# Kernel tuning notes

Measured on AMD Instinct MI355X. Metric: run time of the kernel, lower is better.

Reference implementation:

```python
import jax, jax.numpy as jnp
import numpy as np

B, L, D_MODEL = 4, 2048, 1024
D_INNER = 2 * D_MODEL
D_STATE, DT_RANK = 16, 64
Q = 32768.0  # 2^15 dyadic denominator used by the block


def _find_power_of_2_scale(var, eps=1e-9):
    v = var + eps
    scale = jnp.ones_like(v)
    for t, s in [(4.0, 0.5), (16.0, 0.25), (64.0, 0.125), (256.0, 0.0625),
                 (1024.0, 0.03125), (4096.0, 0.015625), (16384.0, 0.0078125),
                 (65536.0, 0.00390625)]:
        scale = jnp.where(v >= t, s, scale)
    scale = jnp.where(v < 1.0, 1.0, scale)
    scale = jnp.where(v < 0.25, 2.0, scale)
    scale = jnp.where(v < 0.0625, 4.0, scale)
    return scale


def _sigmoid_algebraic(z):
    return 0.5 + 0.5 * z / (1.0 + jnp.abs(z))


def _rsqrt_newton(y, num_iters=3):
    y = jnp.clip(y, 1e-6, 1e6)
    r = jnp.where(y > 16.0, 0.125, 0.5)
    r = jnp.where(y > 64.0, 0.0625, r)
    r = jnp.where(y > 256.0, 0.03125, r)
    r = jnp.where(y < 4.0, 1.0, r)
    r = jnp.where(y < 1.0, 2.0, r)
    r = jnp.where(y < 0.25, 4.0, r)
    for _ in range(num_iters):
        r = jnp.clip(r * (1.5 - 0.5 * y * r * r), 1e-6, 1e3)
    return r


def _squareplus(x):
    y = jnp.clip(x * x + 4.0, 1e-6, 1e6)
    s = jnp.clip(y * _rsqrt_newton(y), 0.0, 1e3)
    return 0.5 * (x + s)


def bitshift_norm(x, gamma, step_size):
    xc = x - x.mean(axis=-1, keepdims=True)
    var = (xc * xc).mean(axis=-1, keepdims=True)
    inv_disc = _find_power_of_2_scale(var)
    inv_diff = jax.lax.rsqrt(var + 1e-6)
    inv = inv_diff + jax.lax.stop_gradient(inv_disc - inv_diff)  # LSQ-style STE
    return xc * inv * gamma * step_size


def bitlinear(x, W):
    # 1.58-bit BitLinear: ternary weight quantization with STE
    s = jnp.mean(jnp.abs(W)) + 1e-8
    Wq = jnp.clip(jnp.round(W / s), -1.0, 1.0) * s
    Wq = W + jax.lax.stop_gradient(Wq - W)
    return x @ Wq.T


def dyadic_scan(u, decay):
    # h[t] = decay[t] * h[t-1] + (1 - decay[t]) * u[t]  (convex combination)
    a = decay
    b = (1.0 - decay) * u
    def comb(c1, c2):
        a1, b1 = c1
        a2, b2 = c2
        return a1 * a2, a2 * b1 + b2
    _, h = jax.lax.associative_scan(comb, (a, b), axis=1)
    return h


def setup_inputs() -> dict:
    key = jax.random.key(0)
    ks = jax.random.split(key, 9)
    d = {}
    d["x"] = jax.random.normal(ks[0], (B, L, D_MODEL), dtype=jnp.float32)
    d["gamma"] = jnp.ones((D_MODEL,), jnp.float32)
    d["step_size"] = jnp.ones((1,), jnp.float32)
    d["W_in"] = jax.random.normal(ks[1], (2 * D_INNER, D_MODEL), jnp.float32) * (D_MODEL ** -0.5)
    d["conv_w"] = jax.random.normal(ks[2], (D_INNER, 1, 4), jnp.float32) * 0.5
    d["conv_b"] = jnp.zeros((D_INNER,), jnp.float32)
    d["W_x"] = jax.random.normal(ks[3], (DT_RANK + 2 * D_STATE, D_INNER), jnp.float32) * (D_INNER ** -0.5)
    d["W_dt"] = jax.random.normal(ks[4], (D_INNER, DT_RANK), jnp.float32) * (DT_RANK ** -0.5)
    d["b_dt"] = jax.random.normal(ks[5], (D_INNER,), jnp.float32) * 0.1
    d["W_out"] = jax.random.normal(ks[6], (D_MODEL, D_INNER), jnp.float32) * (D_INNER ** -0.5)
    return d


def reference(x, gamma, step_size, W_in, conv_w, conv_b, W_x, W_dt, b_dt, W_out):
    Bc, Lc, _ = x.shape
    residual = x
    xn = bitshift_norm(x, gamma, step_size)
    xz = bitlinear(xn, W_in)                      # [B, L, 2*d_inner]
    xc, z = jnp.split(xz, 2, axis=-1)
    # causal depthwise conv1d (kernel 4, torch padding=3, slice back to L)
    xt = xc.transpose(0, 2, 1)                    # [B, d_inner, L]
    y = jax.lax.conv_general_dilated(
        xt, conv_w, (1,), [(3, 3)],
        dimension_numbers=("NCH", "OIH", "NCH"),
        feature_group_count=D_INNER)
    xc = (y[..., :Lc] + conv_b[None, :, None]).transpose(0, 2, 1)
    xc = _squareplus(xc)                          # integer-only activation
    dbl = bitlinear(xc, W_x)                      # [B, L, dt_rank + 2*d_state]
    dt = bitlinear(dbl[..., :DT_RANK], W_dt) + b_dt  # [B, L, d_inner]
    decay_c = _sigmoid_algebraic(dt)
    # dyadic quantization of decay to k/2^15 with STE
    decay = decay_c + jax.lax.stop_gradient(jnp.round(decay_c * Q) / Q - decay_c)
    h = dyadic_scan(xc, decay)                    # [B, L, d_inner]
    y = h * _squareplus(z)
    return bitlinear(y, W_out) + residual
```

## Files before the change

### kernel.cpp

```cpp
#include <hip/hip_runtime.h>
#include <hip/hip_bf16.h>

#define B_ 4
#define L_ 2048
#define DM 1024
#define DI 2048
#define NR (B_ * L_)
#define DTR 64
#define NCHUNK 32
#define CHUNK 64
#define CCONV 64
#define KSLICE 8

typedef __attribute__((ext_vector_type(8))) short short8;
typedef __attribute__((ext_vector_type(4))) float floatx4;

static constexpr size_t OFF_SCAL = 0;
static constexpr size_t OFF_PART = 256;
static constexpr size_t OFF_XN   = 4608;
static constexpr size_t OFF_TIN  = OFF_XN   + (size_t)NR * DM * 2;
static constexpr size_t OFF_TX   = OFF_TIN  + (size_t)2 * DI * DM * 2;
static constexpr size_t OFF_TDT  = OFF_TX   + (size_t)DTR * DI * 2;
static constexpr size_t OFF_TOUT = OFF_TDT  + (size_t)DI * DTR * 2;
static constexpr size_t OFF_XC   = OFF_TOUT + (size_t)DM * DI * 2;
static constexpr size_t OFF_P2   = OFF_XC   + (size_t)NR * DI * 2;
static constexpr size_t OFF_ZSP  = OFF_XC   + (size_t)NR * DI * 4;
static constexpr size_t OFF_XACT = OFF_ZSP  + (size_t)NR * DI * 2;
static constexpr size_t OFF_DBL  = OFF_XACT + (size_t)NR * DI * 2;
static constexpr size_t OFF_DEC  = OFF_DBL  + (size_t)NR * DTR * 2;
static constexpr size_t OFF_CA   = OFF_DEC  + (size_t)NR * DI * 2;
static constexpr size_t OFF_CB   = OFF_CA   + (size_t)B_ * NCHUNK * DI * 4;
static constexpr size_t OFF_Y    = OFF_CB   + (size_t)B_ * NCHUNK * DI * 4;

__device__ __forceinline__ void async16(const void* g, void* l) {
    __builtin_amdgcn_global_load_lds(
        (const __attribute__((address_space(1))) unsigned int*)g,
        (__attribute__((address_space(3))) unsigned int*)l, 16, 0, 0);
}

__device__ __forceinline__ float pow2scale(float var) {
    float v = var + 1e-9f;
    float s = 1.0f;
    if (v >= 4.0f)     s = 0.5f;
    if (v >= 16.0f)    s = 0.25f;
    if (v >= 64.0f)    s = 0.125f;
    if (v >= 256.0f)   s = 0.0625f;
    if (v >= 1024.0f)  s = 0.03125f;
    if (v >= 4096.0f)  s = 0.015625f;
    if (v >= 16384.0f) s = 0.0078125f;
    if (v >= 65536.0f) s = 0.00390625f;
    if (v < 1.0f)    s = 1.0f;
    if (v < 0.25f)   s = 2.0f;
    if (v < 0.0625f) s = 4.0f;
    return s;
}

__device__ __forceinline__ float squareplus_f(float x) {
    float y = fminf(fmaxf(x * x + 4.0f, 1e-6f), 1e6f);
    float r = (y > 16.0f) ? 0.125f : 0.5f;
    if (y > 64.0f)  r = 0.0625f;
    if (y > 256.0f) r = 0.03125f;
    if (y < 4.0f)   r = 1.0f;
    if (y < 1.0f)   r = 2.0f;
    if (y < 0.25f)  r = 4.0f;
#pragma unroll
    for (int i = 0; i < 3; ++i) {
        r = r * (1.5f - 0.5f * y * r * r);
        r = fminf(fmaxf(r, 1e-6f), 1e3f);
    }
    float s = fminf(fmaxf(y * r, 0.0f), 1e3f);
    return 0.5f * (x + s);
}

__device__ __forceinline__ float block_reduce_sum(float v) {
    __shared__ float sm[4];
#pragma unroll
    for (int o = 32; o > 0; o >>= 1) v += __shfl_down(v, o, 64);
    int w = threadIdx.x >> 6;
    __syncthreads();
    if ((threadIdx.x & 63) == 0) sm[w] = v;
    __syncthreads();
    return (sm[0] + sm[1]) + (sm[2] + sm[3]);
}

__global__ __launch_bounds__(256) void k_abs_all(const float* __restrict__ W0,
                                                 const float* __restrict__ W1,
                                                 const float* __restrict__ W2,
                                                 const float* __restrict__ W3,
                                                 float* __restrict__ part) {
    const int w = blockIdx.y;
    const float* W = (w == 0) ? W0 : (w == 1) ? W1 : (w == 2) ? W2 : W3;
    const int n4 = ((w == 0) ? 2 * DI * DM : (w == 1) ? 96 * DI : (w == 2) ? DI * DTR : DM * DI) / 4;
    const float4* W4 = (const float4*)W;
    float s = 0.f;
    for (int i = blockIdx.x * 256 + threadIdx.x; i < n4; i += 256 * 256) {
        float4 v = W4[i];
        s += fabsf(v.x) + fabsf(v.y) + fabsf(v.z) + fabsf(v.w);
    }
    float t = block_reduce_sum(s);
    if (threadIdx.x == 0) part[w * 256 + blockIdx.x] = t;
}

__global__ __launch_bounds__(256) void k_finalize(const float* __restrict__ part,
                                                  float* __restrict__ scal) {
    const float counts[4] = {(float)(2 * DI * DM), (float)(96 * DI),
                             (float)(DI * DTR), (float)(DM * DI)};
    for (int w = 0; w < 4; ++w) {
        float s = block_reduce_sum(part[w * 256 + threadIdx.x]);
        if (threadIdx.x == 0) scal[w] = s / counts[w] + 1e-8f;
    }
}

__global__ __launch_bounds__(256) void k_quant_all(
    const float* __restrict__ W0, const float* __restrict__ W1,
    const float* __restrict__ W2, const float* __restrict__ W3,
    const float* __restrict__ scal,
    __hip_bfloat16* __restrict__ T0, __hip_bfloat16* __restrict__ T1,
    __hip_bfloat16* __restrict__ T2, __hip_bfloat16* __restrict__ T3) {
    int b = blockIdx.x;
    const float* W; const float* sp; __hip_bfloat16* T; int off;
    if (b < 4096)      { W = W0; sp = scal + 0; T = T0; off = b; }
    else if (b < 4224) { W = W1; sp = scal + 1; T = T1; off = b - 4096; }
    else if (b < 4352) { W = W2; sp = scal + 2; T = T2; off = b - 4224; }
    else               { W = W3; sp = scal + 3; T = T3; off = b - 4352; }
    int i = off * 1024 + threadIdx.x * 4;
    float inv = 1.0f / (*sp);
    float4 v = *(const float4*)(W + i);
    __hip_bfloat16 t[4];
    t[0] = __float2bfloat16(fmaxf(-1.0f, fminf(1.0f, rintf(v.x * inv))));
    t[1] = __float2bfloat16(fmaxf(-1.0f, fminf(1.0f, rintf(v.y * inv))));
    t[2] = __float2bfloat16(fmaxf(-1.0f, fminf(1.0f, rintf(v.z * inv))));
    t[3] = __float2bfloat16(fmaxf(-1.0f, fminf(1.0f, rintf(v.w * inv))));
    *reinterpret_cast<uint2*>(&T[i]) = *reinterpret_cast<uint2*>(t);
}

__global__ __launch_bounds__(256) void k_norm(const float* __restrict__ x,
                                              const float* __restrict__ gamma,
                                              const float* __restrict__ step,
                                              __hip_bfloat16* __restrict__ xn) {
    int row = blockIdx.x;
    int tid = threadIdx.x;
    float4 v4 = ((const float4*)(x + (size_t)row * DM))[tid];
    float s = (v4.x + v4.y) + (v4.z + v4.w);
    float mean = block_reduce_sum(s) * (1.0f / DM);
    float d0 = v4.x - mean, d1 = v4.y - mean, d2 = v4.z - mean, d3 = v4.w - mean;
    float vv = d0 * d0 + d1 * d1 + d2 * d2 + d3 * d3;
    float var = block_reduce_sum(vv) * (1.0f / DM);
    float sc = pow2scale(var) * step[0];
    float4 g = ((const float4*)gamma)[tid];
    __hip_bfloat16 t[4];
    t[0] = __float2bfloat16(d0 * sc * g.x);
    t[1] = __float2bfloat16(d1 * sc * g.y);
    t[2] = __float2bfloat16(d2 * sc * g.z);
    t[3] = __float2bfloat16(d3 * sc * g.w);
    *reinterpret_cast<uint2*>(&xn[(size_t)row * DM + tid * 4]) = *reinterpret_cast<uint2*>(t);
}

template <int BM, int BN, int WR, int WC, int MODE>
__global__ __launch_bounds__(256) void k_gemm(
    const __hip_bfloat16* __restrict__ A, const __hip_bfloat16* __restrict__ Bw,
    int M, int N, int K, int lda, int ldb, const float* __restrict__ s_ptr,
    float* __restrict__ o_f32, __hip_bfloat16* __restrict__ o_bf16,
    __hip_bfloat16* __restrict__ o_bf16b, unsigned short* __restrict__ o_u16,
    const float* __restrict__ bias, const float* __restrict__ resid) {
    constexpr int BK = 32;
    constexpr int FM = BM / (WR * 16), FN = BN / (WC * 16);
    constexpr int RA = (BM * BK) / (256 * 8);
    constexpr int RB = (BN * BK) / (256 * 8);
    constexpr int KEEP = RA + RB;
    __shared__ __align__(16) short lA[3][BM * BK];
    __shared__ __align__(16) short lB[3][BN * BK];
    const int tid = threadIdx.x;
    const int lane = tid & 63, wid = tid >> 6;
    const int wm = (wid / WC) * (BM / WR);
    const int wn = (wid % WC) * (BN / WC);
    const int r16 = lane & 15, quad = lane >> 4;

    if (MODE == 4) {
        A  += (size_t)blockIdx.z * K;
        Bw += (size_t)blockIdx.z * K;
        o_f32 += (size_t)blockIdx.z * M * N;
    }

    int nx = gridDim.x;
    int bx = blockIdx.x, by = blockIdx.y;
    if ((nx & 7) == 0 && nx >= 8) {
        int bid = by * nx + bx;
        int xcd = bid & 7, idx = bid >> 3;
        int npx = nx >> 3;
        bx = xcd * npx + (idx % npx);
        by = idx / npx;
    }
    const int m0 = by * BM, n0 = bx * BN;

    floatx4 acc[FM][FN] = {};
    const int NT = K / BK;

#pragma unroll
    for (int r = 0; r < RA; ++r) {
        int idx = r * 256 + tid;
        int row = idx >> 2, kc = (idx & 3) << 3;
        async16(&A[(size_t)(m0 + row) * lda + kc], &lA[0][idx * 8]);
    }
#pragma unroll
    for (int r = 0; r < RB; ++r) {
        int idx = r * 256 + tid;
        int row = idx >> 2, kc = (idx & 3) << 3;
        async16(&Bw[(size_t)(n0 + row) * ldb + kc], &lB[0][idx * 8]);
    }
    if (NT > 1) {
#pragma unroll
        for (int r = 0; r < RA; ++r) {
            int idx = r * 256 + tid;
            int row = idx >> 2, kc = (idx & 3) << 3;
            async16(&A[(size_t)(m0 + row) * lda + BK + kc], &lA[1][idx * 8]);
        }
#pragma unroll
        for (int r = 0; r < RB; ++r) {
            int idx = r * 256 + tid;
            int row = idx >> 2, kc = (idx & 3) << 3;
            async16(&Bw[(size_t)(n0 + row) * ldb + BK + kc], &lB[1][idx * 8]);
        }
    }

    for (int t = 0; t < NT; ++t) {
        if (t > 0) __builtin_amdgcn_s_barrier();
        if (t + 2 < NT) {
            const int k2 = (t + 2) * BK;
            const int nb = (t + 2) % 3;
#pragma unroll
            for (int r = 0; r < RA; ++r) {
                int idx = r * 256 + tid;
                int row = idx >> 2, kc = (idx & 3) << 3;
                async16(&A[(size_t)(m0 + row) * lda + k2 + kc], &lA[nb][idx * 8]);
            }
#pragma unroll
            for (int r = 0; r < RB; ++r) {
                int idx = r * 256 + tid;
                int row = idx >> 2, kc = (idx & 3) << 3;
                async16(&Bw[(size_t)(n0 + row) * ldb + k2 + kc], &lB[nb][idx * 8]);
            }
            __builtin_amdgcn_s_waitcnt(0x0F70 | (2 * KEEP));
        } else if (t + 1 < NT) {
            __builtin_amdgcn_s_waitcnt(0x0F70 | KEEP);
        } else {
            __builtin_amdgcn_s_waitcnt(0x0F70);
        }
        __builtin_amdgcn_s_barrier();

        const int cb = t % 3;
        short8 af[FM], bfv[FN];
#pragma unroll
        for (int i = 0; i < FM; ++i)
            af[i] = *reinterpret_cast<const short8*>(&lA[cb][(wm + i * 16 + r16) * BK + quad * 8]);
#pragma unroll
        for (int j = 0; j < FN; ++j)
            bfv[j] = *reinterpret_cast<const short8*>(&lB[cb][(wn + j * 16 + r16) * BK + quad * 8]);
#pragma unroll
        for (int i = 0; i < FM; ++i)
#pragma unroll
            for (int j = 0; j < FN; ++j)
                acc[i][j] = __builtin_amdgcn_mfma_f32_16x16x32_bf16(af[i], bfv[j], acc[i][j], 0, 0, 0);
    }

    const float s = (MODE == 4) ? 1.0f : *s_ptr;
#pragma unroll
    for (int i = 0; i < FM; ++i) {
#pragma unroll
        for (int j = 0; j < FN; ++j) {
#pragma unroll
            for (int r = 0; r < 4; ++r) {
                int gr = m0 + wm + i * 16 + quad * 4 + r;
                int gc = n0 + wn + j * 16 + r16;
                float v = acc[i][j][r] * s;
                if (MODE == 0) {
                    if (gc < DI) o_bf16[(size_t)gr * DI + gc] = __float2bfloat16(v);
                    else o_bf16b[(size_t)gr * DI + (gc - DI)] = __float2bfloat16(v);
                } else if (MODE == 1) {
                    o_bf16[(size_t)gr * N + gc] = __float2bfloat16(v);
                } else if (MODE == 2) {
                    float dt = v + bias[gc];
                    float dc = 0.5f + 0.5f * dt / (1.0f + fabsf(dt));
                    o_u16[(size_t)gr * N + gc] = (unsigned short)rintf(dc * 32768.0f);
                } else if (MODE == 3) {
                    o_f32[(size_t)gr * N + gc] = v + resid[(size_t)gr * N + gc];
                } else {
                    o_f32[(size_t)gr * N + gc] = v;
                }
            }
        }
    }
}

__global__ __launch_bounds__(256) void k_red(const float* __restrict__ part,
                                             const float* __restrict__ s_ptr,
                                             __hip_bfloat16* __restrict__ dbl) {
    int i = blockIdx.x * 256 + threadIdx.x;
    float s = *s_ptr;
    float acc = 0.f;
#pragma unroll
    for (int z = 0; z < KSLICE; ++z) acc += part[(size_t)z * NR * DTR + i];
    dbl[i] = __float2bfloat16(acc * s);
}

__global__ __launch_bounds__(256) void k_conv(const __hip_bfloat16* __restrict__ xc,
                                              const float* __restrict__ cw,
                                              const float* __restrict__ cb,
                                              __hip_bfloat16* __restrict__ xact) {
    int c = blockIdx.x * 256 + threadIdx.x;
    int t0 = blockIdx.y * CCONV;
    int b = blockIdx.z;
    float w0 = cw[c * 4 + 0], w1 = cw[c * 4 + 1], w2 = cw[c * 4 + 2], w3 = cw[c * 4 + 3];
    float bias = cb[c];
    const __hip_bfloat16* base = xc + (size_t)b * L_ * DI + c;
    float x3 = (t0 - 3 >= 0) ? __bfloat162float(base[(size_t)(t0 - 3) * DI]) : 0.f;
    float x2 = (t0 - 2 >= 0) ? __bfloat162float(base[(size_t)(t0 - 2) * DI]) : 0.f;
    float x1 = (t0 - 1 >= 0) ? __bfloat162float(base[(size_t)(t0 - 1) * DI]) : 0.f;
    for (int t = t0; t < t0 + CCONV; ++t) {
        float xt = __bfloat162float(base[(size_t)t * DI]);
        float y = x3 * w0 + x2 * w1 + x1 * w2 + xt * w3 + bias;
        xact[((size_t)(b * L_ + t)) * DI + c] = __float2bfloat16(squareplus_f(y));
        x3 = x2; x2 = x1; x1 = xt;
    }
}

__global__ __launch_bounds__(256) void k_scan1(const unsigned short* __restrict__ dk,
                                               const __hip_bfloat16* __restrict__ u,
                                               float* __restrict__ cA, float* __restrict__ cB) {
    int c = blockIdx.x * 256 + threadIdx.x;
    int j = blockIdx.y, b = blockIdx.z;
    size_t base = ((size_t)b * L_ + (size_t)j * CHUNK) * DI + c;
    float Ac = 1.f, Bc = 0.f;
    for (int t = 0; t < CHUNK; ++t) {
        float a = dk[base + (size_t)t * DI] * (1.0f / 32768.0f);
        float uv = __bfloat162float(u[base + (size_t)t * DI]);
        Bc = a * Bc + (1.f - a) * uv;
        Ac *= a;
    }
    size_t o = ((size_t)(b * NCHUNK + j)) * DI + c;
    cA[o] = Ac;
    cB[o] = Bc;
}

__global__ __launch_bounds__(256) void k_scan3(const unsigned short* __restrict__ dk,
                                               const __hip_bfloat16* __restrict__ u,
                                               const __hip_bfloat16* __restrict__ zraw,
                                               const float* __restrict__ cA,
                                               const float* __restrict__ cB,
                                               __hip_bfloat16* __restrict__ y) {
    int c = blockIdx.x * 256 + threadIdx.x;
    int j = blockIdx.y, b = blockIdx.z;
    float h = 0.f;
    for (int jj = 0; jj < j; ++jj) {
        size_t o = ((size_t)(b * NCHUNK + jj)) * DI + c;
        h = cA[o] * h + cB[o];
    }
    size_t base = ((size_t)b * L_ + (size_t)j * CHUNK) * DI + c;
    for (int t = 0; t < CHUNK; ++t) {
        float a = dk[base + (size_t)t * DI] * (1.0f / 32768.0f);
        float uv = __bfloat162float(u[base + (size_t)t * DI]);
        h = a * h + (1.f - a) * uv;
        float zv = squareplus_f(__bfloat162float(zraw[base + (size_t)t * DI]));
        y[base + (size_t)t * DI] = __float2bfloat16(h * zv);
    }
}

extern "C" void kernel_launch(void* const* d_in, const int* in_sizes, int n_in,
                              void* d_out, int out_size, void* d_ws, size_t ws_size,
                              hipStream_t stream) {
    const float* x      = (const float*)d_in[0];
    const float* gamma  = (const float*)d_in[1];
    const float* step   = (const float*)d_in[2];
    const float* W_in   = (const float*)d_in[3];
    const float* conv_w = (const float*)d_in[4];
    const float* conv_b = (const float*)d_in[5];
    const float* W_x    = (const float*)d_in[6];
    const float* W_dt   = (const float*)d_in[7];
    const float* b_dt   = (const float*)d_in[8];
    const float* W_out  = (const float*)d_in[9];

    char* ws = (char*)d_ws;
    float*          scal = (float*)(ws + OFF_SCAL);
    float*          part = (float*)(ws + OFF_PART);
    __hip_bfloat16* xn   = (__hip_bfloat16*)(ws + OFF_XN);
    __hip_bfloat16* Tin  = (__hip_bfloat16*)(ws + OFF_TIN);
    __hip_bfloat16* Tx   = (__hip_bfloat16*)(ws + OFF_TX);
    __hip_bfloat16* Tdt  = (__hip_bfloat16*)(ws + OFF_TDT);
    __hip_bfloat16* Tout = (__hip_bfloat16*)(ws + OFF_TOUT);
    __hip_bfloat16* xcb  = (__hip_bfloat16*)(ws + OFF_XC);
    float*          p2   = (float*)(ws + OFF_P2);
    __hip_bfloat16* zraw = (__hip_bfloat16*)(ws + OFF_ZSP);
    __hip_bfloat16* xact = (__hip_bfloat16*)(ws + OFF_XACT);
    __hip_bfloat16* dbl  = (__hip_bfloat16*)(ws + OFF_DBL);
    unsigned short* dec  = (unsigned short*)(ws + OFF_DEC);
    float*          cA   = (float*)(ws + OFF_CA);
    float*          cB   = (float*)(ws + OFF_CB);
    __hip_bfloat16* yb   = (__hip_bfloat16*)(ws + OFF_Y);
    float*          out  = (float*)d_out;

    k_abs_all<<<dim3(256, 4), 256, 0, stream>>>(W_in, W_x, W_dt, W_out, part);
    k_finalize<<<1, 256, 0, stream>>>(part, scal);
    k_quant_all<<<6400, 256, 0, stream>>>(W_in, W_x, W_dt, W_out, scal, Tin, Tx, Tdt, Tout);

    k_norm<<<NR, 256, 0, stream>>>(x, gamma, step, xn);

    k_gemm<128, 128, 2, 2, 0><<<dim3((2 * DI) / 128, NR / 128), 256, 0, stream>>>(
        xn, Tin, NR, 2 * DI, DM, DM, DM, scal + 0, nullptr, xcb, zraw, nullptr, nullptr, nullptr);

    k_conv<<<dim3(DI / 256, L_ / CCONV, B_), 256, 0, stream>>>(xcb, conv_w, conv_b, xact);

    k_gemm<64, 64, 2, 2, 4><<<dim3(1, NR / 64, KSLICE), 256, 0, stream>>>(
        xact, Tx, NR, DTR, DI / KSLICE, DI, DI, nullptr, p2, nullptr, nullptr, nullptr, nullptr, nullptr);
    k_red<<<(NR * DTR) / 256, 256, 0, stream>>>(p2, scal + 1, dbl);

    k_gemm<128, 128, 2, 2, 2><<<dim3(DI / 128, NR / 128), 256, 0, stream>>>(
        dbl, Tdt, NR, DI, DTR, DTR, DTR, scal + 2, nullptr, nullptr, nullptr, dec, b_dt, nullptr);

    k_scan1<<<dim3(DI / 256, NCHUNK, B_), 256, 0, stream>>>(dec, xact, cA, cB);
    k_scan3<<<dim3(DI / 256, NCHUNK, B_), 256, 0, stream>>>(dec, xact, zraw, cA, cB, yb);

    k_gemm<64, 128, 2, 2, 3><<<dim3(DM / 128, NR / 64), 256, 0, stream>>>(
        yb, Tout, NR, DM, DI, DI, DI, scal + 3, out, nullptr, nullptr, nullptr, nullptr, x);

    (void)in_sizes; (void)n_in; (void)out_size; (void)ws_size;
}
```

Baseline: 377.0 us.

## Run input projection GEMM in int8 MFMA with per-row activation scaling

Stores the ternary W_in as packed int8 and quantizes the normalized activations to int8 with a per-row absmax scale. A new int8 GEMM kernel uses i32 16x16x64 MFMA and applies the weight and row scales in the epilogue. This halves operand bytes and doubles MFMA throughput for the largest GEMM, but adds activation quantization error that the bf16 path did not have. The dt GEMM tile is also changed from 128x128 to 64x128.

Result: faster. 343.6 us (-8.8%).

```diff
diff --git a/kernel.cpp b/kernel.cpp
--- a/kernel.cpp
+++ b/kernel.cpp
@@ -14,6 +14,7 @@
 
 typedef __attribute__((ext_vector_type(8))) short short8;
 typedef __attribute__((ext_vector_type(4))) float floatx4;
+typedef __attribute__((ext_vector_type(4))) int int4v;
 
 static constexpr size_t OFF_SCAL = 0;
 static constexpr size_t OFF_PART = 256;
@@ -31,6 +32,7 @@
 static constexpr size_t OFF_CA   = OFF_DEC  + (size_t)NR * DI * 2;
 static constexpr size_t OFF_CB   = OFF_CA   + (size_t)B_ * NCHUNK * DI * 4;
 static constexpr size_t OFF_Y    = OFF_CB   + (size_t)B_ * NCHUNK * DI * 4;
+static constexpr size_t OFF_SROW = OFF_Y    + (size_t)NR * DI * 2;
 
 __device__ __forceinline__ void async16(const void* g, void* l) {
     __builtin_amdgcn_global_load_lds(
@@ -83,6 +85,17 @@
     return (sm[0] + sm[1]) + (sm[2] + sm[3]);
 }
 
+__device__ __forceinline__ float block_reduce_max(float v) {
+    __shared__ float smx[4];
+#pragma unroll
+    for (int o = 32; o > 0; o >>= 1) v = fmaxf(v, __shfl_down(v, o, 64));
+    int w = threadIdx.x >> 6;
+    __syncthreads();
+    if ((threadIdx.x & 63) == 0) smx[w] = v;
+    __syncthreads();
+    return fmaxf(fmaxf(smx[0], smx[1]), fmaxf(smx[2], smx[3]));
+}
+
 __global__ __launch_bounds__(256) void k_abs_all(const float* __restrict__ W0,
                                                  const float* __restrict__ W1,
                                                  const float* __restrict__ W2,
@@ -115,12 +128,23 @@
     const float* __restrict__ W0, const float* __restrict__ W1,
     const float* __restrict__ W2, const float* __restrict__ W3,
     const float* __restrict__ scal,
-    __hip_bfloat16* __restrict__ T0, __hip_bfloat16* __restrict__ T1,
+    signed char* __restrict__ T0, __hip_bfloat16* __restrict__ T1,
     __hip_bfloat16* __restrict__ T2, __hip_bfloat16* __restrict__ T3) {
     int b = blockIdx.x;
+    if (b < 4096) {
+        int i = b * 1024 + threadIdx.x * 4;
+        float inv = 1.0f / scal[0];
+        float4 v = *(const float4*)(W0 + i);
+        int q0 = (int)fmaxf(-1.0f, fminf(1.0f, rintf(v.x * inv)));
+        int q1 = (int)fmaxf(-1.0f, fminf(1.0f, rintf(v.y * inv)));
+        int q2 = (int)fmaxf(-1.0f, fminf(1.0f, rintf(v.z * inv)));
+        int q3 = (int)fmaxf(-1.0f, fminf(1.0f, rintf(v.w * inv)));
+        unsigned int packed = (q0 & 255) | ((q1 & 255) << 8) | ((q2 & 255) << 16) | ((q3 & 255) << 24);
+        *reinterpret_cast<unsigned int*>(&T0[i]) = packed;
+        return;
+    }
     const float* W; const float* sp; __hip_bfloat16* T; int off;
-    if (b < 4096)      { W = W0; sp = scal + 0; T = T0; off = b; }
-    else if (b < 4224) { W = W1; sp = scal + 1; T = T1; off = b - 4096; }
+    if (b < 4224)      { W = W1; sp = scal + 1; T = T1; off = b - 4096; }
     else if (b < 4352) { W = W2; sp = scal + 2; T = T2; off = b - 4224; }
     else               { W = W3; sp = scal + 3; T = T3; off = b - 4352; }
     int i = off * 1024 + threadIdx.x * 4;
@@ -137,7 +161,8 @@
 __global__ __launch_bounds__(256) void k_norm(const float* __restrict__ x,
                                               const float* __restrict__ gamma,
                                               const float* __restrict__ step,
-                                              __hip_bfloat16* __restrict__ xn) {
+                                              signed char* __restrict__ xn8,
+                                              float* __restrict__ srow) {
     int row = blockIdx.x;
     int tid = threadIdx.x;
     float4 v4 = ((const float4*)(x + (size_t)row * DM))[tid];
@@ -148,12 +173,118 @@
     float var = block_reduce_sum(vv) * (1.0f / DM);
     float sc = pow2scale(var) * step[0];
     float4 g = ((const float4*)gamma)[tid];
-    __hip_bfloat16 t[4];
-    t[0] = __float2bfloat16(d0 * sc * g.x);
-    t[1] = __float2bfloat16(d1 * sc * g.y);
-    t[2] = __float2bfloat16(d2 * sc * g.z);
-    t[3] = __float2bfloat16(d3 * sc * g.w);
-    *reinterpret_cast<uint2*>(&xn[(size_t)row * DM + tid * 4]) = *reinterpret_cast<uint2*>(t);
+    float w0 = d0 * sc * g.x, w1 = d1 * sc * g.y, w2 = d2 * sc * g.z, w3 = d3 * sc * g.w;
+    float am = fmaxf(fmaxf(fabsf(w0), fabsf(w1)), fmaxf(fabsf(w2), fabsf(w3)));
+    am = block_reduce_max(am);
+    float sr = (am > 0.f) ? am * (1.0f / 127.0f) : 1.0f;
+    float inv = 1.0f / sr;
+    if (tid == 0) srow[row] = sr;
+    int q0 = (int)rintf(w0 * inv), q1 = (int)rintf(w1 * inv);
+    int q2 = (int)rintf(w2 * inv), q3 = (int)rintf(w3 * inv);
+    unsigned int packed = (q0 & 255) | ((q1 & 255) << 8) | ((q2 & 255) << 16) | ((q3 & 255) << 24);
+    ((unsigned int*)xn8)[row * 256 + tid] = packed;
+}
+
+__global__ __launch_bounds__(256) void k_gemm1_i8(
+    const signed char* __restrict__ A, const signed char* __restrict__ Bw,
+    const float* __restrict__ s_ptr, const float* __restrict__ srow,
+    __hip_bfloat16* __restrict__ o_xc, __hip_bfloat16* __restrict__ o_z) {
+    constexpr int BM = 128, BN = 128, BKB = 64;
+    constexpr int FM = 4, FN = 4;
+    constexpr int RA = 2, RB = 2, KEEP = RA + RB;
+    constexpr int K = DM, NT = K / 64;
+    __shared__ __align__(16) signed char lA[3][BM * BKB];
+    __shared__ __align__(16) signed char lB[3][BN * BKB];
+    const int tid = threadIdx.x;
+    const int lane = tid & 63, wid = tid >> 6;
+    const int wm = (wid >> 1) * 64;
+    const int wn = (wid & 1) * 64;
+    const int r16 = lane & 15, quad = lane >> 4;
+
+    int nx = gridDim.x;
+    int bx = blockIdx.x, by = blockIdx.y;
+    {
+        int bid = by * nx + bx;
+        int xcd = bid & 7, idx = bid >> 3;
+        int npx = nx >> 3;
+        bx = xcd * npx + (idx % npx);
+        by = idx / npx;
+    }
+    const int m0 = by * BM, n0 = bx * BN;
+
+    int4v acc[FM][FN] = {};
+
+#pragma unroll
+    for (int p = 0; p < 2; ++p) {
+#pragma unroll
+        for (int r = 0; r < RA; ++r) {
+            int idx = r * 256 + tid;
+            int row = idx >> 2, kc = (idx & 3) << 4;
+            async16(&A[(size_t)(m0 + row) * K + p * 64 + kc], &lA[p][idx * 16]);
+        }
+#pragma unroll
+        for (int r = 0; r < RB; ++r) {
+            int idx = r * 256 + tid;
+            int row = idx >> 2, kc = (idx & 3) << 4;
+            async16(&Bw[(size_t)(n0 + row) * K + p * 64 + kc], &lB[p][idx * 16]);
+        }
+    }
+
+    for (int t = 0; t < NT; ++t) {
+        if (t > 0) __builtin_amdgcn_s_barrier();
+        if (t + 2 < NT) {
+            const int k2 = (t + 2) * 64;
+            const int nb = (t + 2) % 3;
+#pragma unroll
+            for (int r = 0; r < RA; ++r) {
+                int idx = r * 256 + tid;
+                int row = idx >> 2, kc = (idx & 3) << 4;
+                async16(&A[(size_t)(m0 + row) * K + k2 + kc], &lA[nb][idx * 16]);
+            }
+#pragma unroll
+            for (int r = 0; r < RB; ++r) {
+                int idx = r * 256 + tid;
+                int row = idx >> 2, kc = (idx & 3) << 4;
+                async16(&Bw[(size_t)(n0 + row) * K + k2 + kc], &lB[nb][idx * 16]);
+            }
+            __builtin_amdgcn_s_waitcnt(0x0F70 | (2 * KEEP));
+        } else if (t + 1 < NT) {
+            __builtin_amdgcn_s_waitcnt(0x0F70 | KEEP);
+        } else {
+            __builtin_amdgcn_s_waitcnt(0x0F70);
+        }
+        __builtin_amdgcn_s_barrier();
+
+        const int cb = t % 3;
+        int4v af[FM], bfv[FN];
+#pragma unroll
+        for (int i = 0; i < FM; ++i)
+            af[i] = *reinterpret_cast<const int4v*>(&lA[cb][(wm + i * 16 + r16) * BKB + quad * 16]);
+#pragma unroll
+        for (int j = 0; j < FN; ++j)
+            bfv[j] = *reinterpret_cast<const int4v*>(&lB[cb][(wn + j * 16 + r16) * BKB + quad * 16]);
+#pragma unroll
+        for (int i = 0; i < FM; ++i)
+#pragma unroll
+            for (int j = 0; j < FN; ++j)
+                acc[i][j] = __builtin_amdgcn_mfma_i32_16x16x64_i8(af[i], bfv[j], acc[i][j], 0, 0, 0);
+    }
+
+    const float sW = *s_ptr;
+#pragma unroll
+    for (int i = 0; i < FM; ++i) {
+#pragma unroll
+        for (int j = 0; j < FN; ++j) {
+#pragma unroll
+            for (int r = 0; r < 4; ++r) {
+                int gr = m0 + wm + i * 16 + quad * 4 + r;
+                int gc = n0 + wn + j * 16 + r16;
+                float v = (float)acc[i][j][r] * sW * srow[gr];
+                if (gc < DI) o_xc[(size_t)gr * DI + gc] = __float2bfloat16(v);
+                else         o_z[(size_t)gr * DI + (gc - DI)] = __float2bfloat16(v);
+            }
+        }
+    }
 }
 
 template <int BM, int BN, int WR, int WC, int MODE>
@@ -161,7 +292,7 @@
     const __hip_bfloat16* __restrict__ A, const __hip_bfloat16* __restrict__ Bw,
     int M, int N, int K, int lda, int ldb, const float* __restrict__ s_ptr,
     float* __restrict__ o_f32, __hip_bfloat16* __restrict__ o_bf16,
-    __hip_bfloat16* __restrict__ o_bf16b, unsigned short* __restrict__ o_u16,
+    unsigned short* __restrict__ o_u16,
     const float* __restrict__ bias, const float* __restrict__ resid) {
     constexpr int BK = 32;
     constexpr int FM = BM / (WR * 16), FN = BN / (WC * 16);
@@ -273,10 +404,7 @@
                 int gr = m0 + wm + i * 16 + quad * 4 + r;
                 int gc = n0 + wn + j * 16 + r16;
                 float v = acc[i][j][r] * s;
-                if (MODE == 0) {
-                    if (gc < DI) o_bf16[(size_t)gr * DI + gc] = __float2bfloat16(v);
-                    else o_bf16b[(size_t)gr * DI + (gc - DI)] = __float2bfloat16(v);
-                } else if (MODE == 1) {
+                if (MODE == 1) {
                     o_bf16[(size_t)gr * N + gc] = __float2bfloat16(v);
                 } else if (MODE == 2) {
                     float dt = v + bias[gc];
@@ -382,8 +510,8 @@
     char* ws = (char*)d_ws;
     float*          scal = (float*)(ws + OFF_SCAL);
     float*          part = (float*)(ws + OFF_PART);
-    __hip_bfloat16* xn   = (__hip_bfloat16*)(ws + OFF_XN);
-    __hip_bfloat16* Tin  = (__hip_bfloat16*)(ws + OFF_TIN);
+    signed char*    xn8  = (signed char*)(ws + OFF_XN);
+    signed char*    Tin8 = (signed char*)(ws + OFF_TIN);
     __hip_bfloat16* Tx   = (__hip_bfloat16*)(ws + OFF_TX);
     __hip_bfloat16* Tdt  = (__hip_bfloat16*)(ws + OFF_TDT);
     __hip_bfloat16* Tout = (__hip_bfloat16*)(ws + OFF_TOUT);
@@ -396,31 +524,32 @@
     float*          cA   = (float*)(ws + OFF_CA);
     float*          cB   = (float*)(ws + OFF_CB);
     __hip_bfloat16* yb   = (__hip_bfloat16*)(ws + OFF_Y);
+    float*          srow = (float*)(ws + OFF_SROW);
     float*          out  = (float*)d_out;
 
     k_abs_all<<<dim3(256, 4), 256, 0, stream>>>(W_in, W_x, W_dt, W_out, part);
     k_finalize<<<1, 256, 0, stream>>>(part, scal);
-    k_quant_all<<<6400, 256, 0, stream>>>(W_in, W_x, W_dt, W_out, scal, Tin, Tx, Tdt, Tout);
-
-    k_norm<<<NR, 256, 0, stream>>>(x, gamma, step, xn);
-
-    k_gemm<128, 128, 2, 2, 0><<<dim3((2 * DI) / 128, NR / 128), 256, 0, stream>>>(
-        xn, Tin, NR, 2 * DI, DM, DM, DM, scal + 0, nullptr, xcb, zraw, nullptr, nullptr, nullptr);
+    k_quant_all<<<6400, 256, 0, stream>>>(W_in, W_x, W_dt, W_out, scal, Tin8, Tx, Tdt, Tout);
+
+    k_norm<<<NR, 256, 0, stream>>>(x, gamma, step, xn8, srow);
+
+    k_gemm1_i8<<<dim3((2 * DI) / 128, NR / 128), 256, 0, stream>>>(
+        xn8, Tin8, scal + 0, srow, xcb, zraw);
 
     k_conv<<<dim3(DI / 256, L_ / CCONV, B_), 256, 0, stream>>>(xcb, conv_w, conv_b, xact);
 
     k_gemm<64, 64, 2, 2, 4><<<dim3(1, NR / 64, KSLICE), 256, 0, stream>>>(
-        xact, Tx, NR, DTR, DI / KSLICE, DI, DI, nullptr, p2, nullptr, nullptr, nullptr, nullptr, nullptr);
+        xact, Tx, NR, DTR, DI / KSLICE, DI, DI, nullptr, p2, nullptr, nullptr, nullptr, nullptr);
     k_red<<<(NR * DTR) / 256, 256, 0, stream>>>(p2, scal + 1, dbl);
 
-    k_gemm<128, 128, 2, 2, 2><<<dim3(DI / 128, NR / 128), 256, 0, stream>>>(
-        dbl, Tdt, NR, DI, DTR, DTR, DTR, scal + 2, nullptr, nullptr, nullptr, dec, b_dt, nullptr);
+    k_gemm<64, 128, 2, 2, 2><<<dim3(DI / 128, NR / 64), 256, 0, stream>>>(
+        dbl, Tdt, NR, DI, DTR, DTR, DTR, scal + 2, nullptr, nullptr, dec, b_dt, nullptr);
 
     k_scan1<<<dim3(DI / 256, NCHUNK, B_), 256, 0, stream>>>(dec, xact, cA, cB);
     k_scan3<<<dim3(DI / 256, NCHUNK, B_), 256, 0, stream>>>(dec, xact, zraw, cA, cB, yb);
 
     k_gemm<64, 128, 2, 2, 3><<<dim3(DM / 128, NR / 64), 256, 0, stream>>>(
-        yb, Tout, NR, DM, DI, DI, DI, scal + 3, out, nullptr, nullptr, nullptr, nullptr, x);
+        yb, Tout, NR, DM, DI, DI, DI, scal + 3, out, nullptr, nullptr, nullptr, x);
 
     (void)in_sizes; (void)n_in; (void)out_size; (void)ws_size;
 }
```
